# Optimization experiments

Measured on AMD Instinct MI355X. Metric: run time of the kernel, lower is better.

The kernel has to match this reference:

```python
import jax, jax.numpy as jnp
import numpy as np

# --- static config (matches init_kwargs) ---
D_MODEL = 1024
EXPAND = 2
D_INNER = EXPAND * D_MODEL          # 2048
D_STATE = 16
DT_RANK = (D_MODEL + 15) // 16      # 64 ('auto')
EPS = 1e-5                          # norm_eps
FP_ITERS = 8                        # max_iter (fixed-count fixed-point iteration)
STEP = 0.99                         # FixedPointOptimizer initial stepsize (damping)
B_SZ, L_SEQ = 2, 2048


def setup_inputs() -> dict:
    key = jax.random.key(0)
    ks = jax.random.split(key, 12)
    f32 = jnp.float32
    hidden_states = jax.random.normal(ks[0], (B_SZ, L_SEQ, D_MODEL), f32)
    # parameters (weight_norm layers represented by their effective weight matrices)
    W_in = jax.random.normal(ks[1], (2 * D_INNER, D_MODEL), f32) * (D_MODEL ** -0.5)
    W_x = jax.random.normal(ks[2], (DT_RANK + 2 * D_STATE, D_INNER), f32) * (D_INNER ** -0.5)
    W_dt = jax.random.uniform(ks[3], (D_INNER, DT_RANK), f32, -DT_RANK ** -0.5, DT_RANK ** -0.5)
    # dt bias: inverse-softplus of dt sampled log-uniform in [dt_min, dt_max]
    dt = jnp.exp(jax.random.uniform(ks[4], (D_INNER,), f32) * (np.log(0.1) - np.log(0.001)) + np.log(0.001))
    dt = jnp.clip(dt, 1e-4)
    b_dt = dt + jnp.log(-jnp.expm1(-dt))
    A_log = jnp.log(jnp.tile(jnp.arange(1, D_STATE + 1, dtype=f32)[None, :], (D_INNER, 1)))
    W_bc = jax.random.normal(ks[5], (2 * D_STATE, D_INNER), f32) * (D_INNER ** -0.5)
    W_zy = jax.random.normal(ks[6], (D_INNER, D_INNER), f32) * (D_INNER ** -0.5)
    W_mix = jax.random.normal(ks[7], (D_INNER, D_INNER), f32) * (D_INNER ** -0.5)
    D = jnp.ones((D_INNER,), f32)
    ln_gamma = jnp.ones((D_INNER,), f32)
    ln_beta = jnp.zeros((D_INNER,), f32)
    W_out = jax.random.normal(ks[8], (D_MODEL, D_INNER), f32) * (D_INNER ** -0.5)
    return dict(hidden_states=hidden_states, W_in=W_in, W_x=W_x, W_dt=W_dt, b_dt=b_dt,
                A_log=A_log, W_bc=W_bc, W_zy=W_zy, W_mix=W_mix, D=D,
                ln_gamma=ln_gamma, ln_beta=ln_beta, W_out=W_out)


def _shift1(y):
    # shift(y, 1, dim=1): causal shift along sequence, zero-fill at t=0
    return jnp.pad(y, ((0, 0), (1, 0), (0, 0)))[:, :-1, :]


def _selective_scan(u, delta, A, Bm, Cm, D):
    # u, delta: (b,l,d); Bm, Cm: (b,l,n); A: (d,n); D: (d,)
    def step(h, inp):
        dt_t, u_t, b_t, c_t = inp  # (b,d),(b,d),(b,n),(b,n)
        h = jnp.exp(dt_t[:, :, None] * A) * h + (dt_t * u_t)[:, :, None] * b_t[:, None, :]
        y = jnp.einsum('bdn,bn->bd', h, c_t) + D * u_t
        return h, y
    b, l, d = u.shape
    h0 = jnp.zeros((b, d, A.shape[1]), u.dtype)
    xs = tuple(jnp.moveaxis(a, 1, 0) for a in (delta, u, Bm, Cm))
    _, ys = jax.lax.scan(step, h0, xs)
    return jnp.moveaxis(ys, 0, 1)  # (b,l,d)


def reference(hidden_states, W_in, W_x, W_dt, b_dt, A_log, W_bc, W_zy, W_mix, D, ln_gamma, ln_beta, W_out):
    # --- _prepare_components ---
    xz = hidden_states @ W_in.T                       # (b,l,2*d_inner)
    x, z = xz[..., :D_INNER], xz[..., D_INNER:]
    x_dbl = x @ W_x.T                                 # (b,l,dt_rank+2n)
    dt_low = x_dbl[..., :DT_RANK]
    B0 = x_dbl[..., DT_RANK:DT_RANK + D_STATE]
    C0 = x_dbl[..., DT_RANK + D_STATE:]
    delta = jax.nn.softplus(dt_low @ W_dt.T + b_dt)   # delta_bias + delta_softplus
    A = -jnp.exp(A_log)

    def layer_norm(y):
        m = jnp.mean(y, -1, keepdims=True)
        v = jnp.var(y, -1, keepdims=True)
        return ln_gamma * (y - m) * jax.lax.rsqrt(v + EPS) + ln_beta

    def bc_normalize(v):  # F.normalize over d_state axis
        n = jnp.linalg.norm(v, axis=-1, keepdims=True)
        return v / jnp.maximum(n, EPS)

    def fp_step(y_prev):
        # channel mixing (NonSelective mixer: learned linear map on delta_x)
        x_tilde = (x - y_prev) @ W_mix.T + y_prev
        bc = _shift1(y_prev) @ W_bc.T                 # bc_y_proj of shifted y
        Bt = bc_normalize(B0 + bc[..., :D_STATE])
        Ct = bc_normalize(C0 + bc[..., D_STATE:])
        y = _selective_scan(x_tilde, delta, A, Bt, Ct, D)
        return layer_norm(y)

    # --- fixed-point iteration (no_grad in original) with damped updates ---
    y0 = jnp.zeros_like(x)
    y_star = jax.lax.fori_loop(0, FP_ITERS, lambda i, y: y + STEP * (fp_step(y) - y), y0)
    y_star = jax.lax.stop_gradient(y_star)
    # --- n_backwards=1 differentiable step ---
    y = fp_step(y_star)
    # --- output gating (glu_in_loop=False path) ---
    z2 = z + _shift1(y) @ W_zy.T
    return (jax.nn.silu(z2) * y) @ W_out.T            # (b,l,d_model)
```

## Files before the change

kernel.cpp:

```cpp
#include <hip/hip_runtime.h>
#include <math.h>

#define B_SZ   2
#define LSEQ   2048
#define DM     1024
#define DI     2048
#define NST    16
#define DTR    64
#define XDBL_N 96
#define NTOK   (B_SZ * LSEQ)
#define NCH    32
#define CS     64
#define EPSF   1e-5f
#define STEPF  0.99f
#define FP_ITERS 8
#define PKZ    4
#define XKZ    8

typedef __attribute__((ext_vector_type(8))) _Float16 f16x8;
typedef __attribute__((ext_vector_type(4))) float f32x4;
typedef unsigned short ushort_t;

__device__ __forceinline__ ushort_t f2h(float v) {
    _Float16 h = (_Float16)v;
    return __builtin_bit_cast(ushort_t, h);
}
__device__ __forceinline__ float h2f(ushort_t u) {
    return (float)__builtin_bit_cast(_Float16, u);
}
__device__ __forceinline__ void split1(float v, ushort_t& h, ushort_t& l) {
    h = f2h(v);
    l = f2h(v - h2f(h));
}
__device__ __forceinline__ void load_lds16(const void* g, void* l) {
    __builtin_amdgcn_global_load_lds(
        (const __attribute__((address_space(1))) unsigned int*)g,
        (__attribute__((address_space(3))) unsigned int*)l, 16, 0, 0);
}

template <int MODE, int WLO>
__global__ __launch_bounds__(256) void split_bf16(
    const float* __restrict__ A,
    ushort_t* __restrict__ Hi, ushort_t* __restrict__ Lo,
    int M, int K, int lda)
{
    int K4 = K >> 2;
    long total = (long)M * K4;
    for (long i = (long)blockIdx.x * 256 + threadIdx.x; i < total;
         i += (long)gridDim.x * 256) {
        int m = (int)(i / K4);
        int k = (int)(i - (long)m * K4) * 4;
        float4 a;
        if (MODE == 2) {
            int t = m & (LSEQ - 1);
            if (t == 0) a = make_float4(0.f, 0.f, 0.f, 0.f);
            else        a = *(const float4*)(A + (size_t)(m - 1) * lda + k);
        } else {
            a = *(const float4*)(A + (size_t)m * lda + k);
        }
        ushort4 hv, lv;
        split1(a.x, hv.x, lv.x);
        split1(a.y, hv.y, lv.y);
        split1(a.z, hv.z, lv.z);
        split1(a.w, hv.w, lv.w);
        *(ushort4*)(Hi + (size_t)m * K + k) = hv;
        if (WLO)
            *(ushort4*)(Lo + (size_t)m * K + k) = lv;
    }
}

template <int EOP, int NPROD>
__global__ __launch_bounds__(256) void mfma_gemm(
    const ushort_t* __restrict__ Ahi, const ushort_t* __restrict__ Alo,
    const ushort_t* __restrict__ Whi, const ushort_t* __restrict__ Wlo,
    const float* __restrict__ E, const float* __restrict__ E2,
    float* __restrict__ C, ushort_t* __restrict__ Chi, ushort_t* __restrict__ Clo,
    int M, int N, int K, int ldE, int ldE2, int ldc)
{
    constexpr int BK     = 32;
    constexpr int NT     = (NPROD == 1) ? 2 : (NPROD == 2) ? 3 : 4;
    constexpr int TILE_H = 128 * BK;
    constexpr int NISS   = BK / 16;
    __shared__ __align__(16) short lds[2 * NT * TILE_H];
    char* ldsc = (char*)lds;

    const int tid = threadIdx.x, lane = tid & 63, w = tid >> 6;
    const int m0 = blockIdx.y * 128, n0 = blockIdx.x * 128;
    const int wm = (w & 1) * 64, wn = (w >> 1) * 64;

    const int ksub = K / gridDim.z;
    const int kbeg = blockIdx.z * ksub;
    if (gridDim.z > 1) C += (size_t)blockIdx.z * M * ldc;

    f32x4 zero4 = {0.f, 0.f, 0.f, 0.f};
    f32x4 acc[4][4];
    #pragma unroll
    for (int mi = 0; mi < 4; ++mi)
        #pragma unroll
        for (int ni = 0; ni < 4; ++ni) acc[mi][ni] = zero4;

    size_t aoff[NISS], woff[NISS];
    #pragma unroll
    for (int i = 0; i < NISS; ++i) {
        int s   = (w * NISS + i) * 64 + lane;
        int g   = s >> 3, u = s & 7, v = u ^ (g & 7);
        int row = g * 2 + (v >> 2);
        int kc  = (v & 3) * 8;
        aoff[i] = (size_t)(m0 + row) * K + kbeg + kc;
        woff[i] = (size_t)(n0 + row) * K + kbeg + kc;
    }
    const int hb  = (lane & 15) >> 1;
    const int sw  = (((lane & 1) << 2) | (lane >> 4)) ^ hb;
    const int abase = (wm / 2 + hb) * 64 + sw * 8;
    const int bbase = (wn / 2 + hb) * 64 + sw * 8;

    auto stage = [&](int b) {
        char* base = ldsc + b * (NT * TILE_H * 2);
        #pragma unroll
        for (int i = 0; i < NISS; ++i) {
            int dst = (w * NISS + i) * 1024;
            load_lds16(Ahi + aoff[i], base + dst);
            load_lds16(Whi + woff[i], base + TILE_H * 2 + dst);
            if (NPROD >= 2)
                load_lds16(Wlo + woff[i], base + 2 * TILE_H * 2 + dst);
            if (NPROD >= 3)
                load_lds16(Alo + aoff[i], base + 3 * TILE_H * 2 + dst);
            aoff[i] += BK; woff[i] += BK;
        }
    };

    auto compute = [&](int b) {
        const short* sA  = lds + b * NT * TILE_H;
        const short* sW  = sA + TILE_H;
        const short* sWl = sA + 2 * TILE_H;
        const short* sAl = sA + 3 * TILE_H;
        f16x8 ah[4], al[4], bh[4], bl[4];
        #pragma unroll
        for (int mi = 0; mi < 4; ++mi) {
            ah[mi] = *(const f16x8*)(sA + abase + mi * 512);
            if (NPROD >= 3)
                al[mi] = *(const f16x8*)(sAl + abase + mi * 512);
        }
        #pragma unroll
        for (int ni = 0; ni < 4; ++ni) {
            bh[ni] = *(const f16x8*)(sW + bbase + ni * 512);
            if (NPROD >= 2)
                bl[ni] = *(const f16x8*)(sWl + bbase + ni * 512);
        }
        #pragma unroll
        for (int mi = 0; mi < 4; ++mi)
            #pragma unroll
            for (int ni = 0; ni < 4; ++ni) {
                acc[mi][ni] = __builtin_amdgcn_mfma_f32_16x16x32_f16(ah[mi], bh[ni], acc[mi][ni], 0, 0, 0);
                if (NPROD >= 2)
                    acc[mi][ni] = __builtin_amdgcn_mfma_f32_16x16x32_f16(ah[mi], bl[ni], acc[mi][ni], 0, 0, 0);
                if (NPROD >= 3)
                    acc[mi][ni] = __builtin_amdgcn_mfma_f32_16x16x32_f16(al[mi], bh[ni], acc[mi][ni], 0, 0, 0);
            }
    };

    const int nt = ksub / BK;
    stage(0);
    __syncthreads();
    int cur = 0;
    for (int t = 0; t < nt - 1; ++t) {
        stage(cur ^ 1);
        compute(cur);
        __syncthreads();
        cur ^= 1;
    }
    compute(cur);

    const int col = lane & 15, rb = (lane >> 4) * 4;
    #pragma unroll
    for (int mi = 0; mi < 4; ++mi) {
        #pragma unroll
        for (int r = 0; r < 4; ++r) {
            int gm = m0 + wm + mi * 16 + rb + r;
            #pragma unroll
            for (int ni = 0; ni < 4; ++ni) {
                int gn = n0 + wn + ni * 16 + col;
                float v = acc[mi][ni][r];
                if (EOP == 0) {
                    C[(size_t)gm * ldc + gn] = v;
                } else if (EOP == 1) {
                    C[(size_t)gm * ldc + gn] = v + E[(size_t)gm * ldE + gn];
                } else if (EOP == 3) {
                    float z2 = h2f(((const ushort_t*)E)[(size_t)gm * ldE + gn]) + v;
                    float s = 1.f / (1.f + __expf(-z2));
                    float g = z2 * s * E2[(size_t)gm * ldE2 + gn];
                    Chi[(size_t)gm * ldc + gn] = f2h(g);
                } else if (EOP == 10) {
                    Chi[(size_t)gm * ldc + gn] = f2h(v);
                } else if (EOP == 11) {
                    Chi[(size_t)gm * ldc + gn] = f2h(v + E[(size_t)gm * ldE + gn]);
                } else if (EOP == 12) {
                    if (gn < 32) C[(size_t)gm * ldc + gn] = v;
                } else {
                    if (gn < DI) {
                        ushort_t h, l;
                        split1(v, h, l);
                        Chi[(size_t)gm * ldc + gn] = h;
                        Clo[(size_t)gm * ldc + gn] = l;
                    } else {
                        ((ushort_t*)C)[(size_t)gm * ldc + (gn - DI)] = f2h(v);
                    }
                }
            }
        }
    }
}

__global__ __launch_bounds__(256) void transpose_wdt(
    const float* __restrict__ Wdt, float* __restrict__ WdtT)
{
    __shared__ float tile[64][65];
    int r0 = blockIdx.x * 64;
    int tr = threadIdx.x >> 6;
    int tc = threadIdx.x & 63;
    #pragma unroll
    for (int i = 0; i < 16; ++i) {
        int r = tr * 16 + i;
        tile[r][tc] = Wdt[(size_t)(r0 + r) * DTR + tc];
    }
    __syncthreads();
    #pragma unroll
    for (int i = 0; i < 16; ++i) {
        int k = tr * 16 + i;
        WdtT[(size_t)k * DI + r0 + tc] = tile[tc][k];
    }
}

__global__ __launch_bounds__(256) void delta_make(
    const float* __restrict__ xdbl, const float* __restrict__ WdtT,
    const float* __restrict__ bdt, ushort_t* __restrict__ deltah)
{
    __shared__ float sX[4][64];
    const int tok0 = blockIdx.x * 4;
    const int tid = threadIdx.x;
    if (tid < 64) {
        int t = tid >> 4, kc = (tid & 15) * 4;
        *(float4*)&sX[t][kc] =
            *(const float4*)&xdbl[(size_t)(tok0 + t) * XDBL_N + kc];
    }
    __syncthreads();

    const int c0 = tid * 4;
    const int c1 = 1024 + tid * 4;
    float acc[4][8] = {};
    #pragma unroll 2
    for (int k = 0; k < DTR; ++k) {
        float4 w0 = *(const float4*)&WdtT[(size_t)k * DI + c0];
        float4 w1 = *(const float4*)&WdtT[(size_t)k * DI + c1];
        #pragma unroll
        for (int t = 0; t < 4; ++t) {
            float x = sX[t][k];
            acc[t][0] = fmaf(x, w0.x, acc[t][0]);
            acc[t][1] = fmaf(x, w0.y, acc[t][1]);
            acc[t][2] = fmaf(x, w0.z, acc[t][2]);
            acc[t][3] = fmaf(x, w0.w, acc[t][3]);
            acc[t][4] = fmaf(x, w1.x, acc[t][4]);
            acc[t][5] = fmaf(x, w1.y, acc[t][5]);
            acc[t][6] = fmaf(x, w1.z, acc[t][6]);
            acc[t][7] = fmaf(x, w1.w, acc[t][7]);
        }
    }
    float b0[4] = {bdt[c0], bdt[c0 + 1], bdt[c0 + 2], bdt[c0 + 3]};
    float b1[4] = {bdt[c1], bdt[c1 + 1], bdt[c1 + 2], bdt[c1 + 3]};
    #pragma unroll
    for (int t = 0; t < 4; ++t) {
        float v[8];
        #pragma unroll
        for (int j = 0; j < 4; ++j) {
            float a0 = acc[t][j] + b0[j];
            v[j]     = (a0 > 20.f) ? a0 : log1pf(expf(a0));
            float a1 = acc[t][4 + j] + b1[j];
            v[4 + j] = (a1 > 20.f) ? a1 : log1pf(expf(a1));
        }
        ushort_t* d0 = deltah + (size_t)(tok0 + t) * DI + c0;
        ushort_t* d1 = deltah + (size_t)(tok0 + t) * DI + c1;
        *(ushort4*)d0 = make_ushort4(f2h(v[0]), f2h(v[1]), f2h(v[2]), f2h(v[3]));
        *(ushort4*)d1 = make_ushort4(f2h(v[4]), f2h(v[5]), f2h(v[6]), f2h(v[7]));
    }
}

__global__ __launch_bounds__(256) void reduce_xdbl(
    const float* __restrict__ Pd, float* __restrict__ xdbl)
{
    int idx = blockIdx.x * 256 + threadIdx.x;
    if (idx >= NTOK * XDBL_N) return;
    int m = idx / XDBL_N, n = idx - m * XDBL_N;
    float s = 0.f;
    #pragma unroll
    for (int zz = 0; zz < 8; ++zz)
        s += Pd[(size_t)zz * NTOK * 128 + (size_t)m * 128 + n];
    xdbl[(size_t)m * XDBL_N + n] = s;
}

__global__ __launch_bounds__(256) void reduce_xwbc(
    const float* __restrict__ P, float* __restrict__ xWbc)
{
    int idx = blockIdx.x * 256 + threadIdx.x;
    if (idx >= NTOK * 32) return;
    int m = idx >> 5, j = idx & 31;
    float s = 0.f;
    #pragma unroll
    for (int zz = 0; zz < XKZ; ++zz)
        s += P[(size_t)zz * NTOK * 128 + (size_t)m * 128 + j];
    xWbc[(size_t)m * 128 + j] = s;
}

__global__ __launch_bounds__(256) void bc_make(
    const float* __restrict__ xdbl, const float* __restrict__ xWbc,
    const float* __restrict__ Pp, float* __restrict__ Btb, float* __restrict__ Ctb)
{
    int tok = blockIdx.x * 8 + (threadIdx.x >> 5);
    int j = threadIdx.x & 31;
    int t = tok & (LSEQ - 1);
    if (t == LSEQ - 1) return;
    int tn = tok + 1;
    float p = 0.f;
    #pragma unroll
    for (int zz = 0; zz < PKZ; ++zz)
        p += Pp[(size_t)zz * NTOK * 128 + (size_t)tok * 128 + j];
    float v = xdbl[(size_t)tn * XDBL_N + DTR + j]
            + xWbc[(size_t)tok * 128 + j] - p;
    float sq = v * v;
    #pragma unroll
    for (int off = 8; off >= 1; off >>= 1) sq += __shfl_xor(sq, off, 16);
    float nrm = fmaxf(sqrtf(sq), EPSF);
    float outv = v / nrm;
    if (j < 16) Btb[(size_t)tn * NST + j] = outv;
    else        Ctb[(size_t)tn * NST + (j - 16)] = outv;
}

__global__ __launch_bounds__(256) void scan_pass1(
    const ushort_t* __restrict__ delta, const ushort_t* __restrict__ u,
    const float* __restrict__ Bt, const float* __restrict__ Alog,
    float* __restrict__ Ac, float* __restrict__ Hend)
{
    int d = blockIdx.x * 256 + threadIdx.x;
    int c = blockIdx.y, b = blockIdx.z;
    int t0 = c * CS;
    __shared__ float sB[CS][NST];
    for (int i = threadIdx.x; i < CS * NST; i += 256)
        ((float*)sB)[i] = Bt[(size_t)(b * LSEQ + t0) * NST + i];
    __syncthreads();

    float Avals[NST];
    #pragma unroll
    for (int n = 0; n < NST; ++n) Avals[n] = -__expf(Alog[d * NST + n]);
    float h[NST] = {};
    float Pp[NST];
    #pragma unroll
    for (int n = 0; n < NST; ++n) Pp[n] = 1.f;

    const ushort_t* dptr = delta + (size_t)(b * LSEQ + t0) * DI + d;
    const ushort_t* uptr = u + (size_t)(b * LSEQ + t0) * DI + d;
    for (int tt = 0; tt < CS; ++tt) {
        float dt = h2f(dptr[(size_t)tt * DI]);
        float ut = h2f(uptr[(size_t)tt * DI]);
        float wv = dt * ut;
        #pragma unroll
        for (int n = 0; n < NST; ++n) {
            float a = __expf(dt * Avals[n]);
            Pp[n] *= a;
            h[n] = fmaf(a, h[n], wv * sB[tt][n]);
        }
    }
    size_t o = ((size_t)((b * NCH + c) * DI) + d) * NST;
    #pragma unroll
    for (int n = 0; n < NST; ++n) { Ac[o + n] = Pp[n]; Hend[o + n] = h[n]; }
}

__global__ __launch_bounds__(256) void scan_pass2(
    float* __restrict__ Ac, const float* __restrict__ Hend)
{
    int idx = blockIdx.x * 256 + threadIdx.x;
    int b = idx / (DI * NST);
    int dn = idx % (DI * NST);
    float h = 0.f;
    for (int c = 0; c < NCH; ++c) {
        size_t o = (size_t)(b * NCH + c) * DI * NST + dn;
        float a = Ac[o];
        float e = Hend[o];
        Ac[o] = h;
        h = fmaf(a, h, e);
    }
}

__global__ __launch_bounds__(256) void scan_pass3(
    const ushort_t* __restrict__ delta, const ushort_t* __restrict__ u,
    const float* __restrict__ Bt, const float* __restrict__ Ct,
    const float* __restrict__ Alog, const float* __restrict__ Dp,
    const float* __restrict__ Hin, ushort_t* __restrict__ yrawh)
{
    int d = blockIdx.x * 256 + threadIdx.x;
    int c = blockIdx.y, b = blockIdx.z;
    int t0 = c * CS;
    __shared__ float sB[CS][NST];
    __shared__ float sC[CS][NST];
    for (int i = threadIdx.x; i < CS * NST; i += 256) {
        ((float*)sB)[i] = Bt[(size_t)(b * LSEQ + t0) * NST + i];
        ((float*)sC)[i] = Ct[(size_t)(b * LSEQ + t0) * NST + i];
    }
    __syncthreads();

    float Avals[NST];
    #pragma unroll
    for (int n = 0; n < NST; ++n) Avals[n] = -__expf(Alog[d * NST + n]);
    float h[NST];
    size_t o = ((size_t)((b * NCH + c) * DI) + d) * NST;
    #pragma unroll
    for (int n = 0; n < NST; ++n) h[n] = Hin[o + n];
    float Dd = Dp[d];

    const ushort_t* dptr = delta + (size_t)(b * LSEQ + t0) * DI + d;
    const ushort_t* uptr = u + (size_t)(b * LSEQ + t0) * DI + d;
    ushort_t* yptr = yrawh + (size_t)(b * LSEQ + t0) * DI + d;
    for (int tt = 0; tt < CS; ++tt) {
        float dt = h2f(dptr[(size_t)tt * DI]);
        float ut = h2f(uptr[(size_t)tt * DI]);
        float wv = dt * ut;
        float acc = 0.f;
        #pragma unroll
        for (int n = 0; n < NST; ++n) {
            float a = __expf(dt * Avals[n]);
            h[n] = fmaf(a, h[n], wv * sB[tt][n]);
            acc = fmaf(h[n], sC[tt][n], acc);
        }
        yptr[(size_t)tt * DI] = f2h(fmaf(Dd, ut, acc));
    }
}

__global__ __launch_bounds__(256) void ln_update(
    const ushort_t* __restrict__ yrawh, float* __restrict__ ybuf,
    const float* __restrict__ gamma, const float* __restrict__ beta,
    const ushort_t* __restrict__ XHi, const ushort_t* __restrict__ XLo,
    ushort_t* __restrict__ AuHi,
    int is_first, int is_final)
{
    int t = blockIdx.x, b = blockIdx.y;
    int tid = threadIdx.x;
    size_t ro = (size_t)(b * LSEQ + t) * DI;
    const ushort_t* yr = yrawh + ro;
    float* yp = ybuf + ro;

    float s = 0.f, s2 = 0.f;
    float vloc[DI / 256];
    #pragma unroll
    for (int i = 0; i < DI / 256; ++i) {
        float v = h2f(yr[tid + i * 256]);
        vloc[i] = v; s += v; s2 += v * v;
    }
    #pragma unroll
    for (int off = 32; off >= 1; off >>= 1) {
        s += __shfl_down(s, off, 64);
        s2 += __shfl_down(s2, off, 64);
    }
    __shared__ float rs[4], rs2[4];
    __shared__ float smean, srstd;
    int wid = tid >> 6, lane = tid & 63;
    if (lane == 0) { rs[wid] = s; rs2[wid] = s2; }
    __syncthreads();
    if (tid == 0) {
        float S = rs[0] + rs[1] + rs[2] + rs[3];
        float S2 = rs2[0] + rs2[1] + rs2[2] + rs2[3];
        float m = S / (float)DI;
        float var = S2 / (float)DI - m * m;
        smean = m;
        srstd = rsqrtf(var + EPSF);
    }
    __syncthreads();
    float m = smean, r = srstd;

    #pragma unroll
    for (int i = 0; i < DI / 256; ++i) {
        int idx = tid + i * 256;
        float ln = (vloc[i] - m) * r * gamma[idx] + beta[idx];
        float ypv = is_first ? 0.f : yp[idx];
        float yn = is_final ? ln : fmaf(STEPF, ln - ypv, ypv);
        yp[idx] = yn;
        if (!is_final) {
            float xv = h2f(XHi[ro + idx]) + h2f(XLo[ro + idx]);
            AuHi[ro + idx] = f2h(xv - yn);
        }
    }
}

__global__ __launch_bounds__(256) void bc_init(
    const float* __restrict__ xdbl, float* __restrict__ Btb, float* __restrict__ Ctb)
{
    int tok = blockIdx.x * 8 + (threadIdx.x >> 5);
    int i = threadIdx.x & 31;
    float v = xdbl[(size_t)tok * XDBL_N + DTR + i];
    float sq = v * v;
    #pragma unroll
    for (int off = 8; off >= 1; off >>= 1) sq += __shfl_xor(sq, off, 16);
    float nrm = fmaxf(sqrtf(sq), EPSF);
    float outv = v / nrm;
    if (i < 16) Btb[(size_t)tok * NST + i] = outv;
    else        Ctb[(size_t)tok * NST + (i - 16)] = outv;
}

__global__ __launch_bounds__(256) void fill_zero(float* p, size_t n)
{
    size_t i = (size_t)blockIdx.x * blockDim.x + threadIdx.x;
    size_t stride = (size_t)gridDim.x * blockDim.x;
    for (; i < n; i += stride) p[i] = 0.f;
}

extern "C" void kernel_launch(void* const* d_in, const int* in_sizes, int n_in,
                              void* d_out, int out_size, void* d_ws, size_t ws_size,
                              hipStream_t stream)
{
    const float* hs    = (const float*)d_in[0];
    const float* W_in  = (const float*)d_in[1];
    const float* W_x   = (const float*)d_in[2];
    const float* W_dt  = (const float*)d_in[3];
    const float* b_dt  = (const float*)d_in[4];
    const float* A_log = (const float*)d_in[5];
    const float* W_bc  = (const float*)d_in[6];
    const float* W_zy  = (const float*)d_in[7];
    const float* W_mix = (const float*)d_in[8];
    const float* Dp    = (const float*)d_in[9];
    const float* g_ln  = (const float*)d_in[10];
    const float* b_ln  = (const float*)d_in[11];
    const float* W_out = (const float*)d_in[12];
    float* out = (float*)d_out;

    char* ws = (char*)d_ws;
    size_t off = 0;
    auto alloc = [&](size_t bytes) {
        void* p = (void*)(ws + off);
        off += (bytes + 255) & ~(size_t)255;
        return p;
    };
    float*    z      = (float*)alloc((size_t)NTOK * DI * 4);
    ushort_t* XHi    = (ushort_t*)alloc((size_t)NTOK * DI * 2);
    ushort_t* XLo    = (ushort_t*)alloc((size_t)NTOK * DI * 2);
    float*    delta  = (float*)alloc((size_t)NTOK * DI * 4);
    float*    ubuf   = (float*)alloc((size_t)NTOK * DI * 4);
    float*    yA     = (float*)alloc((size_t)NTOK * DI * 4);
    ushort_t* AuHi   = (ushort_t*)alloc((size_t)NTOK * DI * 2);
    ushort_t* AuLo   = (ushort_t*)alloc((size_t)NTOK * DI * 2);
    ushort_t* WmixHi = (ushort_t*)alloc((size_t)DI * DI * 2);
    ushort_t* WmixLo = (ushort_t*)alloc((size_t)DI * DI * 2);
    float*    Ac     = (float*)alloc((size_t)B_SZ * NCH * DI * NST * 4);
    float*    Hend   = (float*)alloc((size_t)B_SZ * NCH * DI * NST * 4);
    float*    xdbl   = (float*)alloc((size_t)NTOK * XDBL_N * 4);
    float*    Btb    = (float*)alloc((size_t)NTOK * NST * 4);
    float*    Ctb    = (float*)alloc((size_t)NTOK * NST * 4);
    float*    Pp     = (float*)alloc((size_t)PKZ * NTOK * 128 * 4);
    float*    xWbc   = (float*)alloc((size_t)NTOK * 128 * 4);
    ushort_t* WbcHi  = (ushort_t*)alloc((size_t)128 * DI * 2);
    ushort_t* WbcLo  = (ushort_t*)alloc((size_t)128 * DI * 2);
    ushort_t* uh     = (ushort_t*)alloc((size_t)NTOK * DI * 2);
    float*    WdtT   = (float*)alloc((size_t)DTR * DI * 4);

    ushort_t* HsHi  = (ushort_t*)ubuf;
    ushort_t* HsLo  = HsHi + (size_t)NTOK * DM;
    ushort_t* WinHi = HsLo + (size_t)NTOK * DM;
    ushort_t* WinLo = WinHi + (size_t)(2 * DI) * DM;
    float*    Pd    = yA;
    float*    xWbcP = yA;
    ushort_t* WxHi  = AuHi;
    ushort_t* WxLo  = WxHi + (size_t)128 * DI;
    ushort_t* deltah = (ushort_t*)delta;
    ushort_t* yrawh  = (ushort_t*)ubuf;
    ushort_t* zh     = (ushort_t*)z;
    ushort_t* Ghi   = (ushort_t*)delta;
    ushort_t* WzyHi = WmixHi;
    ushort_t* WzyLo = WmixLo;
    ushort_t* WoutHi= (ushort_t*)Ac;
    ushort_t* WoutLo= (ushort_t*)Hend;

    dim3 blk(256);

    split_bf16<0, 0><<<4096, blk, 0, stream>>>(hs, HsHi, HsLo, NTOK, DM, DM);
    split_bf16<0, 1><<<4096, blk, 0, stream>>>(W_in, WinHi, WinLo, 2 * DI, DM, DM);
    fill_zero<<<64, blk, 0, stream>>>((float*)WxHi, (size_t)128 * DI / 2);
    fill_zero<<<64, blk, 0, stream>>>((float*)WxLo, (size_t)128 * DI / 2);
    split_bf16<0, 1><<<512, blk, 0, stream>>>(W_x, WxHi, WxLo, XDBL_N, DI, DI);
    split_bf16<0, 1><<<4096, blk, 0, stream>>>(W_mix, WmixHi, WmixLo, DI, DI, DI);
    fill_zero<<<128, blk, 0, stream>>>((float*)WbcHi, (size_t)128 * DI / 2);
    fill_zero<<<128, blk, 0, stream>>>((float*)WbcLo, (size_t)128 * DI / 2);
    split_bf16<0, 1><<<64, blk, 0, stream>>>(W_bc, WbcHi, WbcLo, 32, DI, DI);
    transpose_wdt<<<DI / 64, blk, 0, stream>>>(W_dt, WdtT);

    mfma_gemm<6, 2><<<dim3((2 * DI) / 128, NTOK / 128), blk, 0, stream>>>(
        HsHi, nullptr, WinHi, WinLo, nullptr, nullptr, (float*)zh, XHi, XLo,
        NTOK, 2 * DI, DM, 0, 0, DI);

    mfma_gemm<0, 2><<<dim3(1, NTOK / 128, 8), blk, 0, stream>>>(
        XHi, nullptr, WxHi, WxLo, nullptr, nullptr, Pd, nullptr, nullptr,
        NTOK, 128, DI, 0, 0, 128);
    reduce_xdbl<<<(NTOK * XDBL_N + 255) / 256, blk, 0, stream>>>(Pd, xdbl);

    delta_make<<<NTOK / 4, blk, 0, stream>>>(xdbl, WdtT, b_dt, deltah);

    bc_init<<<NTOK / 8, 256, 0, stream>>>(xdbl, Btb, Ctb);

    mfma_gemm<12, 2><<<dim3(1, NTOK / 128, XKZ), blk, 0, stream>>>(
        XHi, nullptr, WbcHi, WbcLo, nullptr, nullptr, xWbcP, nullptr, nullptr,
        NTOK, 128, DI, 0, 0, 128);
    reduce_xwbc<<<(NTOK * 32 + 255) / 256, blk, 0, stream>>>(xWbcP, xWbc);

    for (int it = 0; it <= FP_ITERS; ++it) {
        const ushort_t* Ah = (it == 0) ? XHi : AuHi;
        if (it == 0) {
            mfma_gemm<10, 1><<<dim3(DI / 128, NTOK / 128), blk, 0, stream>>>(
                Ah, nullptr, WmixHi, WmixLo, nullptr, nullptr, nullptr, uh, nullptr,
                NTOK, DI, DI, 0, 0, DI);
        } else if (it < FP_ITERS) {
            mfma_gemm<11, 1><<<dim3(DI / 128, NTOK / 128), blk, 0, stream>>>(
                Ah, nullptr, WmixHi, WmixLo, yA, nullptr, nullptr, uh, nullptr,
                NTOK, DI, DI, DI, 0, DI);
        } else {
            mfma_gemm<11, 2><<<dim3(DI / 128, NTOK / 128), blk, 0, stream>>>(
                Ah, nullptr, WmixHi, WmixLo, yA, nullptr, nullptr, uh, nullptr,
                NTOK, DI, DI, DI, 0, DI);
        }
        if (it > 0) {
            if (it < FP_ITERS)
                mfma_gemm<12, 1><<<dim3(1, NTOK / 128, PKZ), blk, 0, stream>>>(
                    Ah, nullptr, WbcHi, WbcLo, nullptr, nullptr, Pp, nullptr, nullptr,
                    NTOK, 128, DI, 0, 0, 128);
            else
                mfma_gemm<12, 2><<<dim3(1, NTOK / 128, PKZ), blk, 0, stream>>>(
                    Ah, nullptr, WbcHi, WbcLo, nullptr, nullptr, Pp, nullptr, nullptr,
                    NTOK, 128, DI, 0, 0, 128);
            bc_make<<<NTOK / 8, blk, 0, stream>>>(xdbl, xWbc, Pp, Btb, Ctb);
        }

        scan_pass1<<<dim3(DI / 256, NCH, B_SZ), blk, 0, stream>>>(
            deltah, uh, Btb, A_log, Ac, Hend);
        scan_pass2<<<dim3(B_SZ * DI * NST / 256), blk, 0, stream>>>(Ac, Hend);
        scan_pass3<<<dim3(DI / 256, NCH, B_SZ), blk, 0, stream>>>(
            deltah, uh, Btb, Ctb, A_log, Dp, Ac, yrawh);
        ln_update<<<dim3(LSEQ, B_SZ), blk, 0, stream>>>(
            yrawh, yA, g_ln, b_ln, XHi, XLo, AuHi,
            it == 0 ? 1 : 0, it == FP_ITERS ? 1 : 0);
    }

    split_bf16<2, 0><<<8192, blk, 0, stream>>>(yA, XHi, XLo, NTOK, DI, DI);
    split_bf16<0, 1><<<4096, blk, 0, stream>>>(W_zy, WzyHi, WzyLo, DI, DI, DI);
    mfma_gemm<3, 2><<<dim3(DI / 128, NTOK / 128), blk, 0, stream>>>(
        XHi, nullptr, WzyHi, WzyLo, (const float*)zh, yA, nullptr, Ghi, nullptr,
        NTOK, DI, DI, DI, DI, DI);

    split_bf16<0, 1><<<2048, blk, 0, stream>>>(W_out, WoutHi, WoutLo, DM, DI, DI);
    mfma_gemm<0, 2><<<dim3(DM / 128, NTOK / 128), blk, 0, stream>>>(
        Ghi, nullptr, WoutHi, WoutLo, nullptr, nullptr, out, nullptr, nullptr,
        NTOK, DM, DI, 0, 0, DM);
}
```

Measured before the change: 2.167 ms.

## Triple-buffer GEMM LDS staging with vmcnt waits and drop the third split product

The MFMA GEMM moves from double buffering with `__syncthreads` to a three-stage LDS ring. Each iteration waits on `s_waitcnt vmcnt` for only the oldest stage, then issues a plain barrier, so global-to-LDS loads run further ahead of compute. It also removes the NPROD>=3 term (A-low × W-high), cutting LDS traffic and one MFMA per tile for any kernel that used three products, at some cost in precision. The loop now stages two tiles past the last one, so it reads beyond the K range of the last block. The larger LDS footprint can also lower occupancy.

```diff
diff --git a/kernel.cpp b/kernel.cpp
--- a/kernel.cpp
+++ b/kernel.cpp
@@ -78,10 +78,10 @@
     int M, int N, int K, int ldE, int ldE2, int ldc)
 {
     constexpr int BK     = 32;
-    constexpr int NT     = (NPROD == 1) ? 2 : (NPROD == 2) ? 3 : 4;
+    constexpr int NT     = (NPROD == 1) ? 2 : 3;
     constexpr int TILE_H = 128 * BK;
     constexpr int NISS   = BK / 16;
-    __shared__ __align__(16) short lds[2 * NT * TILE_H];
+    __shared__ __align__(16) short lds[3 * NT * TILE_H];
     char* ldsc = (char*)lds;
 
     const int tid = threadIdx.x, lane = tid & 63, w = tid >> 6;
@@ -123,8 +123,6 @@
             load_lds16(Whi + woff[i], base + TILE_H * 2 + dst);
             if (NPROD >= 2)
                 load_lds16(Wlo + woff[i], base + 2 * TILE_H * 2 + dst);
-            if (NPROD >= 3)
-                load_lds16(Alo + aoff[i], base + 3 * TILE_H * 2 + dst);
             aoff[i] += BK; woff[i] += BK;
         }
     };
@@ -133,14 +131,10 @@
         const short* sA  = lds + b * NT * TILE_H;
         const short* sW  = sA + TILE_H;
         const short* sWl = sA + 2 * TILE_H;
-        const short* sAl = sA + 3 * TILE_H;
-        f16x8 ah[4], al[4], bh[4], bl[4];
-        #pragma unroll
-        for (int mi = 0; mi < 4; ++mi) {
+        f16x8 ah[4], bh[4], bl[4];
+        #pragma unroll
+        for (int mi = 0; mi < 4; ++mi)
             ah[mi] = *(const f16x8*)(sA + abase + mi * 512);
-            if (NPROD >= 3)
-                al[mi] = *(const f16x8*)(sAl + abase + mi * 512);
-        }
         #pragma unroll
         for (int ni = 0; ni < 4; ++ni) {
             bh[ni] = *(const f16x8*)(sW + bbase + ni * 512);
@@ -154,22 +148,24 @@
                 acc[mi][ni] = __builtin_amdgcn_mfma_f32_16x16x32_f16(ah[mi], bh[ni], acc[mi][ni], 0, 0, 0);
                 if (NPROD >= 2)
                     acc[mi][ni] = __builtin_amdgcn_mfma_f32_16x16x32_f16(ah[mi], bl[ni], acc[mi][ni], 0, 0, 0);
-                if (NPROD >= 3)
-                    acc[mi][ni] = __builtin_amdgcn_mfma_f32_16x16x32_f16(al[mi], bh[ni], acc[mi][ni], 0, 0, 0);
             }
     };
 
     const int nt = ksub / BK;
     stage(0);
-    __syncthreads();
-    int cur = 0;
-    for (int t = 0; t < nt - 1; ++t) {
-        stage(cur ^ 1);
-        compute(cur);
-        __syncthreads();
-        cur ^= 1;
-    }
-    compute(cur);
+    stage(1);
+    int bufc = 0, bufs = 2;
+    for (int t = 0; t < nt; ++t) {
+        if constexpr (NPROD == 1)
+            asm volatile("s_waitcnt vmcnt(4)" ::: "memory");
+        else
+            asm volatile("s_waitcnt vmcnt(6)" ::: "memory");
+        __builtin_amdgcn_s_barrier();
+        stage(bufs);
+        compute(bufc);
+        bufc = (bufc == 2) ? 0 : bufc + 1;
+        bufs = (bufs == 2) ? 0 : bufs + 1;
+    }
 
     const int col = lane & 15, rb = (lane >> 4) * 4;
     #pragma unroll
```

Result: faster. 1.965 ms (-9.4%).
